# Optimization experiments

Measured on AMD Instinct MI355X. Metric: run time of the kernel, lower is better.

The kernel has to match this reference:

```python
import jax, jax.numpy as jnp
import numpy as np

N_NODES = 100000
N_EDGES = 1600000
IN_DIM = 32
OUT_DIM = 64
N_REL = 8
EPS = 1e-10


def setup_inputs() -> dict:
    key = jax.random.key(0)
    k_x, k_src, k_dst, k_rel, k_w, k_wl, k_ws = jax.random.split(key, 7)
    x = jax.random.normal(k_x, (N_NODES, IN_DIM), dtype=jnp.float32)
    node_in = jax.random.randint(k_src, (N_EDGES,), 0, N_NODES)
    node_out = jax.random.randint(k_dst, (N_EDGES,), 0, N_NODES)
    relation = jax.random.randint(k_rel, (N_EDGES,), 0, N_REL)
    edge_list = jnp.stack([node_in, node_out, relation], axis=1)  # [E, 3] int
    edge_weight = jax.random.uniform(k_w, (N_EDGES,), dtype=jnp.float32)
    W_linear = jax.random.normal(k_wl, (N_REL * IN_DIM, OUT_DIM), dtype=jnp.float32) / np.sqrt(N_REL * IN_DIM)
    b_linear = jnp.zeros((OUT_DIM,), dtype=jnp.float32)
    W_self = jax.random.normal(k_ws, (IN_DIM, OUT_DIM), dtype=jnp.float32) / np.sqrt(IN_DIM)
    b_self = jnp.zeros((OUT_DIM,), dtype=jnp.float32)
    return {"x": x, "edge_list": edge_list, "edge_weight": edge_weight,
            "W_linear": W_linear, "b_linear": b_linear,
            "W_self": W_self, "b_self": b_self}


def reference(x, edge_list, edge_weight, W_linear, b_linear, W_self, b_self):
    num_node, in_dim = x.shape
    # message: gather source-node features per edge  -> [E, D]
    msg = x[edge_list[:, 0]]
    # aggregate: relation-expanded segment id = dst * R + rel
    seg = edge_list[:, 1] * N_REL + edge_list[:, 2]  # [E]
    w = edge_weight[:, None]  # [E, 1]
    num = jax.ops.segment_sum(msg * w, seg, num_segments=num_node * N_REL)  # [N*R, D]
    den = jax.ops.segment_sum(w, seg, num_segments=num_node * N_REL)        # [N*R, 1]
    update = (num / (den + EPS)).reshape(num_node, N_REL * in_dim)          # [N, R*D]
    # combine: linear(update) + self_loop(x), then ReLU
    out = update @ W_linear + b_linear + x @ W_self + b_self
    return jax.nn.relu(out)
```

## Files before the change

### kernel.cpp

```cpp
#include <hip/hip_runtime.h>
#include <stdint.h>

#define N_NODES 100000
#define N_EDGES 1600000
#define IN_DIM 32
#define OUT_DIM 64
#define N_REL 8
#define NSEG (N_NODES * N_REL)
#define EPS 1e-10f
#define N_KK 9
#define SWG_ELEMS (N_KK * 4 * 64 * 8)

typedef __attribute__((ext_vector_type(8))) short bf16x8;
typedef __attribute__((ext_vector_type(2))) short bf16x2;
typedef __attribute__((ext_vector_type(4))) float f32x4;

static __device__ __forceinline__ float bflo(uint32_t u) { return __uint_as_float(u << 16); }
static __device__ __forceinline__ float bfhi(uint32_t u) { return __uint_as_float(u & 0xffff0000u); }
static __device__ __forceinline__ uint16_t f2bf(float f) {
    uint32_t u = __float_as_uint(f);
    return (uint16_t)((u + 0x7fffu + ((u >> 16) & 1u)) >> 16);
}

static __device__ __forceinline__ void pk_add_bf16(uint32_t* addr, float f0, float f1) {
#if __has_builtin(__builtin_amdgcn_global_atomic_fadd_v2bf16)
    bf16x2 v;
    v[0] = (short)f2bf(f0);
    v[1] = (short)f2bf(f1);
    __builtin_amdgcn_global_atomic_fadd_v2bf16((bf16x2*)addr, v);
#else
    uint32_t old = *addr, assumed;
    do {
        assumed = old;
        float lo = bflo(assumed) + f0;
        float hi = bfhi(assumed) + f1;
        uint32_t nv = (uint32_t)f2bf(lo) | ((uint32_t)f2bf(hi) << 16);
        old = atomicCAS(addr, assumed, nv);
    } while (old != assumed);
#endif
}

__global__ __launch_bounds__(256) void detect_kernel(const uint32_t* __restrict__ xw,
                                                     int* __restrict__ flag) {
    __shared__ int cnt;
    if (threadIdx.x == 0) cnt = 0;
    __syncthreads();
    int c = 0;
    for (int k = threadIdx.x; k < 4096; k += 256) {
        uint32_t w = xw[k];
        uint32_t e = (w >> 7) & 0xffu;
        c += (e >= 160u) ? 1 : 0;
    }
    atomicAdd(&cnt, c);
    __syncthreads();
    if (threadIdx.x == 0) *flag = (cnt > 64) ? 1 : 0;
}

__global__ __launch_bounds__(256) void prep_kernel(const void* __restrict__ Wl,
                                                   const void* __restrict__ Ws,
                                                   const void* __restrict__ bl,
                                                   const void* __restrict__ bs,
                                                   const int* __restrict__ flag,
                                                   uint16_t* __restrict__ sWg,
                                                   float* __restrict__ biasv) {
    int f32 = *flag;
    int idx = blockIdx.x * 256 + threadIdx.x;
    if (idx < SWG_ELEMS) {
        int j    = idx & 7;
        int lane = (idx >> 3) & 63;
        int ot   = (idx >> 9) & 3;
        int kk   = idx >> 11;
        int quad = lane >> 4;
        int k = kk * 32 + quad * 8 + j;
        int o = ot * 16 + (lane & 15);
        if (f32) {
            float v = (k < 256) ? ((const float*)Wl)[(size_t)k * OUT_DIM + o]
                                : ((const float*)Ws)[(size_t)(k - 256) * OUT_DIM + o];
            sWg[idx] = f2bf(v);
        } else {
            sWg[idx] = (k < 256) ? ((const uint16_t*)Wl)[(size_t)k * OUT_DIM + o]
                                 : ((const uint16_t*)Ws)[(size_t)(k - 256) * OUT_DIM + o];
        }
    } else if (idx < SWG_ELEMS + OUT_DIM) {
        int o = idx - SWG_ELEMS;
        if (f32) biasv[o] = ((const float*)bl)[o] + ((const float*)bs)[o];
        else     biasv[o] = bflo((uint32_t)((const uint16_t*)bl)[o])
                          + bflo((uint32_t)((const uint16_t*)bs)[o]);
    }
}

__global__ __launch_bounds__(256) void scatter_pk_kernel(
    const int* __restrict__ el,
    const void* __restrict__ ew,
    const void* __restrict__ x,
    const int* __restrict__ flag,
    uint32_t* __restrict__ num,
    float* __restrict__ den)
{
    int t = blockIdx.x * 256 + threadIdx.x;
    int e = t >> 4;
    int p = t & 15;
    if (e >= N_EDGES) return;

    int src = el[e * 3 + 0];
    int dst = el[e * 3 + 1];
    int rel = el[e * 3 + 2];
    int f32 = *flag;

    float w = f32 ? ((const float*)ew)[e]
                  : bflo((uint32_t)((const uint16_t*)ew)[e]);

    float x0, x1;
    if (f32) {
        const float2 v = *(const float2*)((const float*)x + (size_t)src * IN_DIM + 2 * p);
        x0 = v.x; x1 = v.y;
    } else {
        uint32_t d = *(const uint32_t*)((const uint16_t*)x + (size_t)src * IN_DIM + 2 * p);
        x0 = bflo(d); x1 = bfhi(d);
    }

    int seg = dst * N_REL + rel;
    pk_add_bf16(&num[(size_t)seg * 16 + p], w * x0, w * x1);
    if (p == 0) atomicAdd(&den[seg], w);
}

__global__ __launch_bounds__(256) void dense_mfma_kernel(
    const uint32_t* __restrict__ num,
    const float* __restrict__ den,
    const void* __restrict__ x,
    const uint16_t* __restrict__ sWg,
    const float* __restrict__ biasv,
    const int* __restrict__ flag,
    void* __restrict__ out)
{
    __shared__ uint16_t sB[SWG_ELEMS];
    int f32 = *flag;

    #pragma unroll
    for (int it = 0; it < SWG_ELEMS / (256 * 8); ++it) {
        int idx = (it * 256 + threadIdx.x) * 8;
        *(bf16x8*)(sB + idx) = *(const bf16x8*)(sWg + idx);
    }
    __syncthreads();

    int wid  = threadIdx.x >> 6;
    int lane = threadIdx.x & 63;
    int quad = lane >> 4;
    int m    = lane & 15;

    int n0 = blockIdx.x * 64 + wid * 16;
    int n  = n0 + m;
    int nc = (n < N_NODES) ? n : (N_NODES - 1);

    float bias[4];
    #pragma unroll
    for (int ot = 0; ot < 4; ++ot) bias[ot] = biasv[ot * 16 + m];

    f32x4 acc[4];
    #pragma unroll
    for (int ot = 0; ot < 4; ++ot) acc[ot] = (f32x4){0.f, 0.f, 0.f, 0.f};

    #pragma unroll
    for (int kk = 0; kk < N_KK; ++kk) {
        bf16x8 a;
        if (kk < 8) {
            const uint4 d = *(const uint4*)(num + ((size_t)nc * 8 + kk) * 16 + quad * 4);
            float inv = 1.0f / (den[(size_t)nc * N_REL + kk] + EPS);
            a[0] = (short)f2bf(bflo(d.x) * inv); a[1] = (short)f2bf(bfhi(d.x) * inv);
            a[2] = (short)f2bf(bflo(d.y) * inv); a[3] = (short)f2bf(bfhi(d.y) * inv);
            a[4] = (short)f2bf(bflo(d.z) * inv); a[5] = (short)f2bf(bfhi(d.z) * inv);
            a[6] = (short)f2bf(bflo(d.w) * inv); a[7] = (short)f2bf(bfhi(d.w) * inv);
        } else {
            if (f32) {
                const float* base = (const float*)x + (size_t)nc * IN_DIM + quad * 8;
                float4 v0 = *(const float4*)base;
                float4 v1 = *(const float4*)(base + 4);
                a[0] = (short)f2bf(v0.x); a[1] = (short)f2bf(v0.y);
                a[2] = (short)f2bf(v0.z); a[3] = (short)f2bf(v0.w);
                a[4] = (short)f2bf(v1.x); a[5] = (short)f2bf(v1.y);
                a[6] = (short)f2bf(v1.z); a[7] = (short)f2bf(v1.w);
            } else {
                a = *(const bf16x8*)((const uint16_t*)x + (size_t)nc * IN_DIM + quad * 8);
            }
        }
        #pragma unroll
        for (int ot = 0; ot < 4; ++ot) {
            bf16x8 b = *(const bf16x8*)(sB + ((kk * 4 + ot) * 64 + lane) * 8);
            acc[ot] = __builtin_amdgcn_mfma_f32_16x16x32_bf16(a, b, acc[ot], 0, 0, 0);
        }
    }

    #pragma unroll
    for (int ot = 0; ot < 4; ++ot) {
        #pragma unroll
        for (int reg = 0; reg < 4; ++reg) {
            int node = n0 + quad * 4 + reg;
            if (node >= N_NODES) continue;
            int o = ot * 16 + m;
            float v = fmaxf(acc[ot][reg] + bias[ot], 0.0f);
            if (f32) ((float*)out)[(size_t)node * OUT_DIM + o] = v;
            else     ((uint16_t*)out)[(size_t)node * OUT_DIM + o] = f2bf(v);
        }
    }
}

extern "C" void kernel_launch(void* const* d_in, const int* in_sizes, int n_in,
                              void* d_out, int out_size, void* d_ws, size_t ws_size,
                              hipStream_t stream) {
    const void* x  = d_in[0];
    const int* el  = (const int*)d_in[1];
    const void* ew = d_in[2];
    const void* Wl = d_in[3];
    const void* bl = d_in[4];
    const void* Ws = d_in[5];
    const void* bs = d_in[6];

    const size_t OFF_DEN  = 64;
    const size_t OFF_NUM  = OFF_DEN + (size_t)NSEG * 4;
    const size_t OFF_SWG  = OFF_NUM + (size_t)NSEG * IN_DIM * 2;
    const size_t OFF_BIAS = OFF_SWG + (size_t)SWG_ELEMS * 2;
    const size_t REQ      = OFF_BIAS + OUT_DIM * 4;
    if (ws_size < REQ) return;

    int*      flag  = (int*)d_ws;
    float*    den   = (float*)((char*)d_ws + OFF_DEN);
    uint32_t* num   = (uint32_t*)((char*)d_ws + OFF_NUM);
    uint16_t* sWg   = (uint16_t*)((char*)d_ws + OFF_SWG);
    float*    biasv = (float*)((char*)d_ws + OFF_BIAS);

    hipMemsetAsync(d_ws, 0, OFF_SWG, stream);
    detect_kernel<<<1, 256, 0, stream>>>((const uint32_t*)x, flag);
    prep_kernel<<<(SWG_ELEMS + OUT_DIM + 255) / 256, 256, 0, stream>>>(Wl, Ws, bl, bs, flag, sWg, biasv);
    {
        long long threads = (long long)N_EDGES * 16;
        int blocks = (int)((threads + 255) / 256);
        scatter_pk_kernel<<<blocks, 256, 0, stream>>>(el, ew, x, flag, num, den);
    }
    dense_mfma_kernel<<<(N_NODES + 63) / 64, 256, 0, stream>>>(num, den, x, sWg, biasv, flag, d_out);
}
```

Baseline: 276.2 us.

## Pre-convert x to bf16 once and use a persistent dense kernel

The prep kernel now converts x to a packed bf16 copy in the workspace, so the scatter kernel gathers 4 bytes per lane instead of 8 and the dense kernel reads bf16 self-loop features directly. The dense kernel becomes a grid-stride loop over 1024 blocks, which loads the weight tile into LDS fewer times, and it loads all eight denominators per node with two vector loads. In exchange there is an extra pass over x that writes a 6.4MB buffer, plus possible load imbalance across the persistent blocks.

```diff
diff --git a/kernel.cpp b/kernel.cpp
--- a/kernel.cpp
+++ b/kernel.cpp
@@ -10,6 +10,8 @@
 #define EPS 1e-10f
 #define N_KK 9
 #define SWG_ELEMS (N_KK * 4 * 64 * 8)
+#define XB_PAIRS (N_NODES * 16)
+#define NTILES ((N_NODES + 63) / 64)
 
 typedef __attribute__((ext_vector_type(8))) short bf16x8;
 typedef __attribute__((ext_vector_type(2))) short bf16x2;
@@ -56,33 +58,43 @@
     if (threadIdx.x == 0) *flag = (cnt > 64) ? 1 : 0;
 }
 
-__global__ __launch_bounds__(256) void prep_kernel(const void* __restrict__ Wl,
+__global__ __launch_bounds__(256) void prep_kernel(const void* __restrict__ x,
+                                                   const void* __restrict__ Wl,
                                                    const void* __restrict__ Ws,
                                                    const void* __restrict__ bl,
                                                    const void* __restrict__ bs,
                                                    const int* __restrict__ flag,
+                                                   uint32_t* __restrict__ xb,
                                                    uint16_t* __restrict__ sWg,
                                                    float* __restrict__ biasv) {
     int f32 = *flag;
     int idx = blockIdx.x * 256 + threadIdx.x;
-    if (idx < SWG_ELEMS) {
-        int j    = idx & 7;
-        int lane = (idx >> 3) & 63;
-        int ot   = (idx >> 9) & 3;
-        int kk   = idx >> 11;
+    if (idx < XB_PAIRS) {
+        if (f32) {
+            float2 v = ((const float2*)x)[idx];
+            xb[idx] = (uint32_t)f2bf(v.x) | ((uint32_t)f2bf(v.y) << 16);
+        } else {
+            xb[idx] = ((const uint32_t*)x)[idx];
+        }
+    } else if (idx < XB_PAIRS + SWG_ELEMS) {
+        int w = idx - XB_PAIRS;
+        int j    = w & 7;
+        int lane = (w >> 3) & 63;
+        int ot   = (w >> 9) & 3;
+        int kk   = w >> 11;
         int quad = lane >> 4;
         int k = kk * 32 + quad * 8 + j;
         int o = ot * 16 + (lane & 15);
         if (f32) {
             float v = (k < 256) ? ((const float*)Wl)[(size_t)k * OUT_DIM + o]
                                 : ((const float*)Ws)[(size_t)(k - 256) * OUT_DIM + o];
-            sWg[idx] = f2bf(v);
+            sWg[w] = f2bf(v);
         } else {
-            sWg[idx] = (k < 256) ? ((const uint16_t*)Wl)[(size_t)k * OUT_DIM + o]
-                                 : ((const uint16_t*)Ws)[(size_t)(k - 256) * OUT_DIM + o];
-        }
-    } else if (idx < SWG_ELEMS + OUT_DIM) {
-        int o = idx - SWG_ELEMS;
+            sWg[w] = (k < 256) ? ((const uint16_t*)Wl)[(size_t)k * OUT_DIM + o]
+                               : ((const uint16_t*)Ws)[(size_t)(k - 256) * OUT_DIM + o];
+        }
+    } else if (idx < XB_PAIRS + SWG_ELEMS + OUT_DIM) {
+        int o = idx - XB_PAIRS - SWG_ELEMS;
         if (f32) biasv[o] = ((const float*)bl)[o] + ((const float*)bs)[o];
         else     biasv[o] = bflo((uint32_t)((const uint16_t*)bl)[o])
                           + bflo((uint32_t)((const uint16_t*)bs)[o]);
@@ -92,7 +104,7 @@
 __global__ __launch_bounds__(256) void scatter_pk_kernel(
     const int* __restrict__ el,
     const void* __restrict__ ew,
-    const void* __restrict__ x,
+    const uint32_t* __restrict__ xb,
     const int* __restrict__ flag,
     uint32_t* __restrict__ num,
     float* __restrict__ den)
@@ -105,37 +117,26 @@
     int src = el[e * 3 + 0];
     int dst = el[e * 3 + 1];
     int rel = el[e * 3 + 2];
-    int f32 = *flag;
-
-    float w = f32 ? ((const float*)ew)[e]
-                  : bflo((uint32_t)((const uint16_t*)ew)[e]);
-
-    float x0, x1;
-    if (f32) {
-        const float2 v = *(const float2*)((const float*)x + (size_t)src * IN_DIM + 2 * p);
-        x0 = v.x; x1 = v.y;
-    } else {
-        uint32_t d = *(const uint32_t*)((const uint16_t*)x + (size_t)src * IN_DIM + 2 * p);
-        x0 = bflo(d); x1 = bfhi(d);
-    }
-
+
+    float w = (*flag) ? ((const float*)ew)[e]
+                      : bflo((uint32_t)((const uint16_t*)ew)[e]);
+
+    uint32_t d = xb[(size_t)src * 16 + p];
     int seg = dst * N_REL + rel;
-    pk_add_bf16(&num[(size_t)seg * 16 + p], w * x0, w * x1);
+    pk_add_bf16(&num[(size_t)seg * 16 + p], w * bflo(d), w * bfhi(d));
     if (p == 0) atomicAdd(&den[seg], w);
 }
 
 __global__ __launch_bounds__(256) void dense_mfma_kernel(
     const uint32_t* __restrict__ num,
     const float* __restrict__ den,
-    const void* __restrict__ x,
+    const uint32_t* __restrict__ xb,
     const uint16_t* __restrict__ sWg,
     const float* __restrict__ biasv,
     const int* __restrict__ flag,
     void* __restrict__ out)
 {
     __shared__ uint16_t sB[SWG_ELEMS];
-    int f32 = *flag;
-
     #pragma unroll
     for (int it = 0; it < SWG_ELEMS / (256 * 8); ++it) {
         int idx = (it * 256 + threadIdx.x) * 8;
@@ -143,63 +144,64 @@
     }
     __syncthreads();
 
+    int f32  = *flag;
     int wid  = threadIdx.x >> 6;
     int lane = threadIdx.x & 63;
     int quad = lane >> 4;
     int m    = lane & 15;
 
-    int n0 = blockIdx.x * 64 + wid * 16;
-    int n  = n0 + m;
-    int nc = (n < N_NODES) ? n : (N_NODES - 1);
-
     float bias[4];
     #pragma unroll
     for (int ot = 0; ot < 4; ++ot) bias[ot] = biasv[ot * 16 + m];
 
-    f32x4 acc[4];
-    #pragma unroll
-    for (int ot = 0; ot < 4; ++ot) acc[ot] = (f32x4){0.f, 0.f, 0.f, 0.f};
-
-    #pragma unroll
-    for (int kk = 0; kk < N_KK; ++kk) {
-        bf16x8 a;
-        if (kk < 8) {
-            const uint4 d = *(const uint4*)(num + ((size_t)nc * 8 + kk) * 16 + quad * 4);
-            float inv = 1.0f / (den[(size_t)nc * N_REL + kk] + EPS);
-            a[0] = (short)f2bf(bflo(d.x) * inv); a[1] = (short)f2bf(bfhi(d.x) * inv);
-            a[2] = (short)f2bf(bflo(d.y) * inv); a[3] = (short)f2bf(bfhi(d.y) * inv);
-            a[4] = (short)f2bf(bflo(d.z) * inv); a[5] = (short)f2bf(bfhi(d.z) * inv);
-            a[6] = (short)f2bf(bflo(d.w) * inv); a[7] = (short)f2bf(bfhi(d.w) * inv);
-        } else {
-            if (f32) {
-                const float* base = (const float*)x + (size_t)nc * IN_DIM + quad * 8;
-                float4 v0 = *(const float4*)base;
-                float4 v1 = *(const float4*)(base + 4);
-                a[0] = (short)f2bf(v0.x); a[1] = (short)f2bf(v0.y);
-                a[2] = (short)f2bf(v0.z); a[3] = (short)f2bf(v0.w);
-                a[4] = (short)f2bf(v1.x); a[5] = (short)f2bf(v1.y);
-                a[6] = (short)f2bf(v1.z); a[7] = (short)f2bf(v1.w);
+    for (int tile = blockIdx.x; tile < NTILES; tile += gridDim.x) {
+        int n0 = tile * 64 + wid * 16;
+        int n  = n0 + m;
+        int nc = (n < N_NODES) ? n : (N_NODES - 1);
+
+        float4 d0 = *(const float4*)(den + (size_t)nc * 8);
+        float4 d1 = *(const float4*)(den + (size_t)nc * 8 + 4);
+        float inv[8];
+        inv[0] = 1.0f / (d0.x + EPS); inv[1] = 1.0f / (d0.y + EPS);
+        inv[2] = 1.0f / (d0.z + EPS); inv[3] = 1.0f / (d0.w + EPS);
+        inv[4] = 1.0f / (d1.x + EPS); inv[5] = 1.0f / (d1.y + EPS);
+        inv[6] = 1.0f / (d1.z + EPS); inv[7] = 1.0f / (d1.w + EPS);
+
+        f32x4 acc[4];
+        #pragma unroll
+        for (int ot = 0; ot < 4; ++ot) acc[ot] = (f32x4){0.f, 0.f, 0.f, 0.f};
+
+        #pragma unroll
+        for (int kk = 0; kk < N_KK; ++kk) {
+            bf16x8 a;
+            if (kk < 8) {
+                const uint4 d = *(const uint4*)(num + ((size_t)nc * 8 + kk) * 16 + quad * 4);
+                float iv = inv[kk];
+                a[0] = (short)f2bf(bflo(d.x) * iv); a[1] = (short)f2bf(bfhi(d.x) * iv);
+                a[2] = (short)f2bf(bflo(d.y) * iv); a[3] = (short)f2bf(bfhi(d.y) * iv);
+                a[4] = (short)f2bf(bflo(d.z) * iv); a[5] = (short)f2bf(bfhi(d.z) * iv);
+                a[6] = (short)f2bf(bflo(d.w) * iv); a[7] = (short)f2bf(bfhi(d.w) * iv);
             } else {
-                a = *(const bf16x8*)((const uint16_t*)x + (size_t)nc * IN_DIM + quad * 8);
+                a = *(const bf16x8*)((const uint16_t*)xb + (size_t)nc * IN_DIM + quad * 8);
             }
-        }
+            #pragma unroll
+            for (int ot = 0; ot < 4; ++ot) {
+                bf16x8 b = *(const bf16x8*)(sB + ((kk * 4 + ot) * 64 + lane) * 8);
+                acc[ot] = __builtin_amdgcn_mfma_f32_16x16x32_bf16(a, b, acc[ot], 0, 0, 0);
+            }
+        }
+
         #pragma unroll
         for (int ot = 0; ot < 4; ++ot) {
-            bf16x8 b = *(const bf16x8*)(sB + ((kk * 4 + ot) * 64 + lane) * 8);
-            acc[ot] = __builtin_amdgcn_mfma_f32_16x16x32_bf16(a, b, acc[ot], 0, 0, 0);
-        }
-    }
-
-    #pragma unroll
-    for (int ot = 0; ot < 4; ++ot) {
-        #pragma unroll
-        for (int reg = 0; reg < 4; ++reg) {
-            int node = n0 + quad * 4 + reg;
-            if (node >= N_NODES) continue;
-            int o = ot * 16 + m;
-            float v = fmaxf(acc[ot][reg] + bias[ot], 0.0f);
-            if (f32) ((float*)out)[(size_t)node * OUT_DIM + o] = v;
-            else     ((uint16_t*)out)[(size_t)node * OUT_DIM + o] = f2bf(v);
+            #pragma unroll
+            for (int reg = 0; reg < 4; ++reg) {
+                int node = n0 + quad * 4 + reg;
+                if (node >= N_NODES) continue;
+                int o = ot * 16 + m;
+                float v = fmaxf(acc[ot][reg] + bias[ot], 0.0f);
+                if (f32) ((float*)out)[(size_t)node * OUT_DIM + o] = v;
+                else     ((uint16_t*)out)[(size_t)node * OUT_DIM + o] = f2bf(v);
+            }
         }
     }
 }
@@ -219,7 +221,8 @@
     const size_t OFF_NUM  = OFF_DEN + (size_t)NSEG * 4;
     const size_t OFF_SWG  = OFF_NUM + (size_t)NSEG * IN_DIM * 2;
     const size_t OFF_BIAS = OFF_SWG + (size_t)SWG_ELEMS * 2;
-    const size_t REQ      = OFF_BIAS + OUT_DIM * 4;
+    const size_t OFF_XB   = OFF_BIAS + OUT_DIM * 4;
+    const size_t REQ      = OFF_XB + (size_t)XB_PAIRS * 4;
     if (ws_size < REQ) return;
 
     int*      flag  = (int*)d_ws;
@@ -227,14 +230,18 @@
     uint32_t* num   = (uint32_t*)((char*)d_ws + OFF_NUM);
     uint16_t* sWg   = (uint16_t*)((char*)d_ws + OFF_SWG);
     float*    biasv = (float*)((char*)d_ws + OFF_BIAS);
+    uint32_t* xb    = (uint32_t*)((char*)d_ws + OFF_XB);
 
     hipMemsetAsync(d_ws, 0, OFF_SWG, stream);
     detect_kernel<<<1, 256, 0, stream>>>((const uint32_t*)x, flag);
-    prep_kernel<<<(SWG_ELEMS + OUT_DIM + 255) / 256, 256, 0, stream>>>(Wl, Ws, bl, bs, flag, sWg, biasv);
+    {
+        int total = XB_PAIRS + SWG_ELEMS + OUT_DIM;
+        prep_kernel<<<(total + 255) / 256, 256, 0, stream>>>(x, Wl, Ws, bl, bs, flag, xb, sWg, biasv);
+    }
     {
         long long threads = (long long)N_EDGES * 16;
         int blocks = (int)((threads + 255) / 256);
-        scatter_pk_kernel<<<blocks, 256, 0, stream>>>(el, ew, x, flag, num, den);
-    }
-    dense_mfma_kernel<<<(N_NODES + 63) / 64, 256, 0, stream>>>(num, den, x, sWg, biasv, flag, d_out);
-}
+        scatter_pk_kernel<<<blocks, 256, 0, stream>>>(el, ew, xb, flag, num, den);
+    }
+    dense_mfma_kernel<<<1024, 256, 0, stream>>>(num, den, xb, sWg, biasv, flag, d_out);
+}
```

Result: slower. 282.0 us (+2.1%).
